# Kernel optimization log

Hardware: AMD Instinct MI355X
Metric: run time of the kernel (lower is better)

Reference implementation:

```python
import jax, jax.numpy as jnp
import numpy as np

# --- dims (match init_kwargs) ---
B = 2048          # batch
BACK = 512        # backcast_length (in_dim of first layer)
UNITS = 512       # hidden units
FORE = 128        # forecast_length
TH = FORE         # thetas_dim (nb_harmonics=None)
NL = 4            # num_block_layers
NUM = 5           # grid intervals
K = 3             # spline order
MINP = 1          # min_period
NCOEF = NUM + K   # 8 spline coefficients per edge


def _grid(in_dim):
    # extended uniform grid over [-1,1] with K extra knots each side -> NUM+2K+1 points
    h = 2.0 / NUM
    pts = (np.arange(-K, NUM + K + 1) * h - 1.0).astype(np.float32)
    return jnp.asarray(np.tile(pts[None, :], (in_dim, 1)))


def _bspline(x, grid):
    # x: (B, in_dim), grid: (in_dim, NUM+2K+1) -> (B, in_dim, NUM+K)
    xe = x[:, :, None]
    g = grid[None]
    v = ((xe >= g[:, :, :-1]) & (xe < g[:, :, 1:])).astype(x.dtype)
    for p in range(1, K + 1):  # Cox-de Boor recursion, K is small & static
        v = (xe - g[:, :, :-(p + 1)]) / (g[:, :, p:-1] - g[:, :, :-(p + 1)]) * v[:, :, :-1] \
          + (g[:, :, p + 1:] - xe) / (g[:, :, p + 1:] - g[:, :, 1:-p]) * v[:, :, 1:]
    return v


def _kan(x, grid, coef, sb, ssp):
    # y[b,o] = sum_i sb[i,o]*silu(x[b,i]) + sum_i ssp[i,o]*sum_k B[b,i,k]*coef[i,o,k]
    # (mask == ones; scale_sp folded into coef to avoid (B,in,out) intermediate)
    bsp = _bspline(x, grid)                          # (B, in, NCOEF)
    base = jax.nn.silu(x)                            # (B, in)
    return base @ sb + jnp.einsum('bik,iok->bo', bsp, coef * ssp[:, :, None])


def _seasonal_basis():
    T = BACK + FORE
    lin = np.linspace(0.0, (T - 1) / T, T)           # linspace(centered=False)
    bl, fl = lin[:BACK], lin[BACK:]
    p1 = p2 = TH // 2                                # TH even
    f1 = np.linspace(0.0, T / MINP, p1)
    f2 = np.linspace(0.0, T / MINP, p2)
    Sb = np.concatenate([np.cos(2 * np.pi * f1[:, None] * bl),
                         np.sin(2 * np.pi * f2[:, None] * bl)]).astype(np.float32)
    Sf = np.concatenate([np.cos(2 * np.pi * f1[:, None] * fl),
                         np.sin(2 * np.pi * f2[:, None] * fl)]).astype(np.float32)
    return jnp.asarray(Sb), jnp.asarray(Sf)          # (TH, BACK), (TH, FORE)


def setup_inputs() -> dict:
    key = jax.random.key(0)
    ks = jax.random.split(key, 8)
    x = jax.random.uniform(ks[0], (B, BACK), jnp.float32, -1.0, 1.0)
    # fc KAN layers: first maps BACK->UNITS, rest UNITS->UNITS; BACK==UNITS so stack
    coef_fc = 0.1 * jax.random.normal(ks[1], (NL, UNITS, UNITS, NCOEF), jnp.float32)
    sb_fc = 0.3 * jax.random.normal(ks[2], (NL, UNITS, UNITS), jnp.float32)
    ssp_fc = 1.0 + 0.1 * jax.random.normal(ks[3], (NL, UNITS, UNITS), jnp.float32)
    # shared theta layer UNITS -> TH
    coef_th = 0.1 * jax.random.normal(ks[4], (UNITS, TH, NCOEF), jnp.float32)
    sb_th = 0.3 * jax.random.normal(ks[5], (UNITS, TH), jnp.float32)
    ssp_th = 1.0 + 0.1 * jax.random.normal(ks[6], (UNITS, TH), jnp.float32)
    return dict(x=x, coef_fc=coef_fc, sb_fc=sb_fc, ssp_fc=ssp_fc,
                coef_th=coef_th, sb_th=sb_th, ssp_th=ssp_th)


def reference(x, coef_fc, sb_fc, ssp_fc, coef_th, sb_th, ssp_th):
    grid = _grid(UNITS)  # BACK == UNITS, one grid serves all layers
    h = x
    for l in range(NL):  # static small layer loop (dropout p=0 / eval)
        h = _kan(h, grid, coef_fc[l], sb_fc[l], ssp_fc[l])
    theta = _kan(h, grid, coef_th, sb_th, ssp_th)  # theta_b_fc is theta_f_fc (shared)
    Sb, Sf = _seasonal_basis()
    backcast = theta @ Sb    # (B, BACK)
    forecast = theta @ Sf    # (B, FORE)
    return backcast, forecast
```

## Files before the change

### kernel.cpp

```cpp
#include <hip/hip_runtime.h>
#include <stdint.h>


typedef unsigned short u16;
typedef __attribute__((ext_vector_type(8))) short short8;
typedef __attribute__((ext_vector_type(4))) float f32x4;

#define NB 2048
#define KD 4608
#define NTH 128
#define NTT 640

__device__ __forceinline__ u16 f2bf(float f) {
  union { float f; uint32_t u; } c; c.f = f;
  return (u16)((c.u + 0x7FFFu + ((c.u >> 16) & 1u)) >> 16);
}

__device__ __forceinline__ void load_lds16(const void* g, void* lds) {
  __builtin_amdgcn_global_load_lds((const __attribute__((address_space(1))) void*)g,
                                   (__attribute__((address_space(3))) void*)lds, 16, 0, 0);
}

__device__ __forceinline__ void bspline8(float x, float* v8) {
  float g[12];
  #pragma unroll
  for (int j = 0; j < 12; ++j) g[j] = (float)((j - 3) * 0.4 - 1.0);
  float w[11];
  #pragma unroll
  for (int j = 0; j < 11; ++j) w[j] = (x >= g[j] && x < g[j+1]) ? 1.0f : 0.0f;
  #pragma unroll
  for (int p = 1; p <= 3; ++p) {
    #pragma unroll
    for (int j = 0; j < 11 - p; ++j) {
      const float i1 = 1.0f / (g[j+p] - g[j]);
      const float i2 = 1.0f / (g[j+p+1] - g[j+1]);
      w[j] = (x - g[j]) * i1 * w[j] + (g[j+p+1] - x) * i2 * w[j+1];
    }
  }
  #pragma unroll
  for (int j = 0; j < 8; ++j) v8[j] = w[j];
}

__device__ __forceinline__ void expand_quad(const float* xv, u16* __restrict__ row, int i0) {
  float base[4], v[4][8];
  #pragma unroll
  for (int e = 0; e < 4; ++e) {
    base[e] = xv[e] / (1.0f + __expf(-xv[e]));
    bspline8(xv[e], v[e]);
  }
  short4 s;
  s.x = (short)f2bf(base[0]); s.y = (short)f2bf(base[1]);
  s.z = (short)f2bf(base[2]); s.w = (short)f2bf(base[3]);
  *(short4*)(row + i0) = s;
  #pragma unroll
  for (int f = 0; f < 8; ++f) {
    s.x = (short)f2bf(v[0][f]); s.y = (short)f2bf(v[1][f]);
    s.z = (short)f2bf(v[2][f]); s.w = (short)f2bf(v[3][f]);
    *(short4*)(row + (1 + f) * 512 + i0) = s;
  }
}

__global__ __launch_bounds__(256)
void setup_kernel(const float* __restrict__ coef_fc, const float* __restrict__ sb_fc,
                  const float* __restrict__ ssp_fc,  const float* __restrict__ coef_th,
                  const float* __restrict__ sb_th,   const float* __restrict__ ssp_th,
                  const float* __restrict__ x,
                  u16* __restrict__ WtFc, u16* __restrict__ WtTh,
                  float* __restrict__ S,  u16* __restrict__ Act) {
  const int blk = blockIdx.x, tid = threadIdx.x;
  __shared__ u16 T[9 * 64 * 66];
  if (blk < 272) {
    const float *coef, *sb, *ssp; u16* Wt; int O, l, i0, o0;
    if (blk < 256) {
      coef = coef_fc; sb = sb_fc; ssp = ssp_fc; Wt = WtFc; O = 512;
      l = blk >> 6; i0 = ((blk >> 3) & 7) * 64; o0 = (blk & 7) * 64;
    } else {
      coef = coef_th; sb = sb_th; ssp = ssp_th; Wt = WtTh; O = 128;
      const int t = blk - 256;
      l = 0; i0 = (t >> 1) * 64; o0 = (t & 1) * 64;
    }
    #pragma unroll 4
    for (int pass = 0; pass < 16; ++pass) {
      const int o_loc = tid & 63;
      const int i_loc = pass * 4 + (tid >> 6);
      const size_t io = ((size_t)l * 512 + i0 + i_loc) * (size_t)O + o0 + o_loc;
      const float sspv = ssp[io];
      const float4 a = *(const float4*)(coef + io * 8);
      const float4 b = *(const float4*)(coef + io * 8 + 4);
      u16* t0 = T + i_loc * 66 + o_loc;
      t0[0 * 64 * 66] = f2bf(sb[io]);
      t0[1 * 64 * 66] = f2bf(a.x * sspv);
      t0[2 * 64 * 66] = f2bf(a.y * sspv);
      t0[3 * 64 * 66] = f2bf(a.z * sspv);
      t0[4 * 64 * 66] = f2bf(a.w * sspv);
      t0[5 * 64 * 66] = f2bf(b.x * sspv);
      t0[6 * 64 * 66] = f2bf(b.y * sspv);
      t0[7 * 64 * 66] = f2bf(b.z * sspv);
      t0[8 * 64 * 66] = f2bf(b.w * sspv);
    }
    __syncthreads();
    #pragma unroll
    for (int f = 0; f < 9; ++f)
      #pragma unroll 4
      for (int pass = 0; pass < 16; ++pass) {
        const int i_loc = tid & 63;
        const int o_loc = pass * 4 + (tid >> 6);
        Wt[((size_t)l * O + o0 + o_loc) * KD + f * 512 + i0 + i_loc] =
            T[(f * 64 + i_loc) * 66 + o_loc];
      }
  } else if (blk < 292) {
    const int base = (blk - 272) * 4096;
    #pragma unroll 4
    for (int q = 0; q < 16; ++q) {
      const int id = base + q * 256 + tid;
      const int j = id & 127, t = id >> 7;
      const int m = ((j & 63) * t) % 63;
      const float ang = (float)(6.283185307179586 * (double)m / 63.0);
      S[(size_t)j * NTT + t] = (j < 64) ? cosf(ang) : sinf(ang);
    }
  } else {
    #pragma unroll
    for (int q = 0; q < 4; ++q) {
      const int qid = (blk - 292) * 1024 + q * 256 + tid;
      const int b = qid >> 7, i0 = (qid & 127) * 4;
      const float4 v = *(const float4*)(x + (size_t)qid * 4);
      float xv[4] = {v.x, v.y, v.z, v.w};
      expand_quad(xv, Act + (size_t)b * KD, i0);
    }
  }
}

template<int NSUM>
__global__ __launch_bounds__(256)
void expand_kernel(const float* __restrict__ src, u16* __restrict__ Act) {
  const int qid = blockIdx.x * 256 + threadIdx.x;
  const int b = qid >> 7, i0 = (qid & 127) * 4;
  float xv[4] = {0.f, 0.f, 0.f, 0.f};
  #pragma unroll
  for (int t = 0; t < NSUM; ++t) {
    const float4 v = *(const float4*)(src + (size_t)t * NB * 512 + (size_t)qid * 4);
    xv[0] += v.x; xv[1] += v.y; xv[2] += v.z; xv[3] += v.w;
  }
  expand_quad(xv, Act + (size_t)b * KD, i0);
}

__device__ __forceinline__ void stage_tile(const u16* __restrict__ A, const u16* __restrict__ Bt,
                                           u16* As, u16* Bs, int rowBase, int colBase,
                                           int kOff, int wave, int lane) {
  const int sRow   = lane >> 3;
  const int sChunk = (lane & 7) ^ sRow;
  #pragma unroll
  for (int j = 0; j < 4; ++j) {
    const int slot = (wave * 4 + j) * 8;
    load_lds16(A  + (size_t)(rowBase + slot + sRow) * KD + kOff + sChunk * 8, As + slot * 64);
    load_lds16(Bt + (size_t)(colBase + slot + sRow) * KD + kOff + sChunk * 8, Bs + slot * 64);
  }
}

__device__ __forceinline__ void mma_step(const u16* As, const u16* Bs, f32x4 acc[4][4],
                                         int wr, int wc, int lane) {
  const int lr = lane & 15, lk8 = lane >> 4;
  #pragma unroll
  for (int ks = 0; ks < 2; ++ks) {
    short8 af[4], bf[4];
    const int kc = ks * 4 + lk8;
    #pragma unroll
    for (int m = 0; m < 4; ++m) {
      const int r = wr * 64 + m * 16 + lr;
      af[m] = *(const short8*)(As + r * 64 + ((kc ^ (r & 7)) * 8));
    }
    #pragma unroll
    for (int n = 0; n < 4; ++n) {
      const int r = wc * 64 + n * 16 + lr;
      bf[n] = *(const short8*)(Bs + r * 64 + ((kc ^ (r & 7)) * 8));
    }
    #pragma unroll
    for (int m = 0; m < 4; ++m)
      #pragma unroll
      for (int n = 0; n < 4; ++n)
        acc[m][n] = __builtin_amdgcn_mfma_f32_16x16x32_bf16(af[m], bf[n], acc[m][n], 0, 0, 0);
  }
}

template<int N, int KITER>
__device__ __forceinline__ void gemm_body(const u16* __restrict__ A, const u16* __restrict__ Bt,
                                          float* __restrict__ Cp, int bx, int by, int bz,
                                          u16* sm) {
  const int tid  = threadIdx.x;
  const int wave = tid >> 6, lane = tid & 63;
  const int rowBase = bx * 128, colBase = by * 128;
  const int kb0 = bz * KITER;
  const int wr = wave >> 1, wc = wave & 1;

  u16 *Ac = sm,             *Bc = sm + 8192;
  u16 *An = sm + 2 * 8192,  *Bn = sm + 3 * 8192;
  u16 *Af = sm + 4 * 8192,  *Bf = sm + 5 * 8192;

  f32x4 acc[4][4] = {};

  stage_tile(A, Bt, Ac, Bc, rowBase, colBase, (kb0 + 0) * 64, wave, lane);
  stage_tile(A, Bt, An, Bn, rowBase, colBase, (kb0 + 1) * 64, wave, lane);

  for (int t = 0; t < KITER - 1; ++t) {
    asm volatile("s_waitcnt vmcnt(8)" ::: "memory");
    __builtin_amdgcn_s_barrier();
    if (t + 2 < KITER)
      stage_tile(A, Bt, Af, Bf, rowBase, colBase, (kb0 + t + 2) * 64, wave, lane);
    mma_step(Ac, Bc, acc, wr, wc, lane);
    __builtin_amdgcn_s_barrier();
    u16* tp;
    tp = Ac; Ac = An; An = Af; Af = tp;
    tp = Bc; Bc = Bn; Bn = Bf; Bf = tp;
  }
  asm volatile("s_waitcnt vmcnt(0)" ::: "memory");
  __builtin_amdgcn_s_barrier();
  mma_step(Ac, Bc, acc, wr, wc, lane);

  float* out = Cp + (size_t)bz * (size_t)NB * N;
  #pragma unroll
  for (int m = 0; m < 4; ++m) {
    const int row0 = rowBase + wr * 64 + m * 16 + (lane >> 4) * 4;
    #pragma unroll
    for (int n = 0; n < 4; ++n) {
      const int col = colBase + wc * 64 + n * 16 + (lane & 15);
      #pragma unroll
      for (int r = 0; r < 4; ++r)
        out[(size_t)(row0 + r) * N + col] = acc[m][n][r];
    }
  }
}

__global__ __launch_bounds__(256, 1)
void gemm_fc(const u16* __restrict__ A, const u16* __restrict__ Bt, float* __restrict__ Cp) {
  __shared__ __align__(16) u16 sm[6 * 8192];
  const int id  = blockIdx.x;
  const int xcd = id & 7;
  const int bz  = xcd >> 1;
  const int u   = id >> 3;
  const int bx  = ((u & 7) << 1) | (xcd & 1);
  const int by  = u >> 3;
  gemm_body<512, 18>(A, Bt, Cp, bx, by, bz, sm);
}

__global__ __launch_bounds__(256, 1)
void gemm_th(const u16* __restrict__ A, const u16* __restrict__ Bt, float* __restrict__ Cp) {
  __shared__ __align__(16) u16 sm[6 * 8192];
  gemm_body<NTH, 9>(A, Bt, Cp, blockIdx.x, 0, blockIdx.z, sm);
}

__global__ __launch_bounds__(256)
void proj_kernel(const float* __restrict__ Part, const float* __restrict__ S,
                 float* __restrict__ out) {
  __shared__ float Ts[64][129];
  const int tid = threadIdx.x;
  const int brow = blockIdx.x * 64, bcol = blockIdx.y * 64;
  for (int idx = tid; idx < 64 * 128; idx += 256) {
    const int r = idx >> 7, c = idx & 127;
    float s = 0.f;
    #pragma unroll
    for (int t = 0; t < 8; ++t)
      s += Part[(size_t)t * NB * NTH + (size_t)(brow + r) * NTH + c];
    Ts[r][c] = s;
  }
  __syncthreads();
  const int tx = tid & 15, ty = tid >> 4;
  const int r0 = ty * 4, c0 = tx * 4;
  float acc[4][4] = {};
  for (int k = 0; k < 128; ++k) {
    const float4 sv = *(const float4*)(S + (size_t)k * NTT + bcol + c0);
    #pragma unroll
    for (int rr = 0; rr < 4; ++rr) {
      const float tv = Ts[r0 + rr][k];
      acc[rr][0] += tv * sv.x; acc[rr][1] += tv * sv.y;
      acc[rr][2] += tv * sv.z; acc[rr][3] += tv * sv.w;
    }
  }
  #pragma unroll
  for (int rr = 0; rr < 4; ++rr) {
    const int b = brow + r0 + rr;
    #pragma unroll
    for (int cc = 0; cc < 4; ++cc) {
      const int t = bcol + c0 + cc;
      if (t < 512) out[(size_t)b * 512 + t] = acc[rr][cc];
      else         out[(size_t)NB * 512 + (size_t)b * NTH + (t - 512)] = acc[rr][cc];
    }
  }
}

extern "C" void kernel_launch(void* const* d_in, const int* in_sizes, int n_in,
                              void* d_out, int out_size, void* d_ws, size_t ws_size,
                              hipStream_t stream) {
  (void)in_sizes; (void)n_in; (void)out_size; (void)ws_size;
  const float* x       = (const float*)d_in[0];
  const float* coef_fc = (const float*)d_in[1];
  const float* sb_fc   = (const float*)d_in[2];
  const float* ssp_fc  = (const float*)d_in[3];
  const float* coef_th = (const float*)d_in[4];
  const float* sb_th   = (const float*)d_in[5];
  const float* ssp_th  = (const float*)d_in[6];
  float* out = (float*)d_out;

  u16*  WtFc = (u16*)d_ws;
  u16*  WtTh = WtFc + (size_t)4 * 512 * KD;
  u16*  Act  = WtTh + (size_t)NTH * KD;
  float* Part = (float*)(Act + (size_t)NB * KD);
  float* S    = Part + (size_t)4 * NB * 512;

  setup_kernel<<<dim3(548), dim3(256), 0, stream>>>(coef_fc, sb_fc, ssp_fc,
                                                    coef_th, sb_th, ssp_th, x,
                                                    WtFc, WtTh, S, Act);
  for (int l = 0; l < 4; ++l) {
    gemm_fc<<<dim3(256), dim3(256), 0, stream>>>(Act, WtFc + (size_t)l * 512 * KD, Part);
    expand_kernel<4><<<dim3(1024), dim3(256), 0, stream>>>(Part, Act);
  }
  gemm_th<<<dim3(16, 1, 8), dim3(256), 0, stream>>>(Act, WtTh, Part);
  proj_kernel<<<dim3(32, 10), dim3(256), 0, stream>>>(Part, S, out);
}
```

Baseline: 240.1 us.

## Fuse B-spline expansion into GEMM epilogue and drop split-K partials

```diff
diff --git a/kernel.cpp b/kernel.cpp
--- a/kernel.cpp
+++ b/kernel.cpp
@@ -130,137 +130,130 @@
   }
 }
 
-template<int NSUM>
-__global__ __launch_bounds__(256)
-void expand_kernel(const float* __restrict__ src, u16* __restrict__ Act) {
-  const int qid = blockIdx.x * 256 + threadIdx.x;
-  const int b = qid >> 7, i0 = (qid & 127) * 4;
-  float xv[4] = {0.f, 0.f, 0.f, 0.f};
-  #pragma unroll
-  for (int t = 0; t < NSUM; ++t) {
-    const float4 v = *(const float4*)(src + (size_t)t * NB * 512 + (size_t)qid * 4);
-    xv[0] += v.x; xv[1] += v.y; xv[2] += v.z; xv[3] += v.w;
-  }
-  expand_quad(xv, Act + (size_t)b * KD, i0);
-}
-
-__device__ __forceinline__ void stage_tile(const u16* __restrict__ A, const u16* __restrict__ Bt,
-                                           u16* As, u16* Bs, int rowBase, int colBase,
-                                           int kOff, int wave, int lane) {
+template<bool EXPAND>
+__global__ __launch_bounds__(512, 1)
+void gemm_fused(const u16* __restrict__ A, const u16* __restrict__ Bt,
+                u16* __restrict__ ActOut, float* __restrict__ ThOut) {
+  __shared__ __align__(16) u16 smb[3 * 8192];
+  __shared__ __align__(16) float Cl[64 * 68];
+  const int tid  = threadIdx.x;
+  const int wave = tid >> 6, lane = tid & 63;
+  int bx, by;
+  if (EXPAND) {
+    const int xcd = blockIdx.x & 7, j = blockIdx.x >> 3;
+    bx = xcd * 4 + (j & 3); by = j >> 2;
+  } else {
+    bx = blockIdx.x & 31; by = blockIdx.x >> 5;
+  }
+  const int rowBase = bx * 64, colBase = by * 64;
+  const int wr = wave >> 2, wc = wave & 3;
+
   const int sRow   = lane >> 3;
   const int sChunk = (lane & 7) ^ sRow;
-  #pragma unroll
-  for (int j = 0; j < 4; ++j) {
-    const int slot = (wave * 4 + j) * 8;
-    load_lds16(A  + (size_t)(rowBase + slot + sRow) * KD + kOff + sChunk * 8, As + slot * 64);
-    load_lds16(Bt + (size_t)(colBase + slot + sRow) * KD + kOff + sChunk * 8, Bs + slot * 64);
-  }
-}
-
-__device__ __forceinline__ void mma_step(const u16* As, const u16* Bs, f32x4 acc[4][4],
-                                         int wr, int wc, int lane) {
-  const int lr = lane & 15, lk8 = lane >> 4;
-  #pragma unroll
-  for (int ks = 0; ks < 2; ++ks) {
-    short8 af[4], bf[4];
-    const int kc = ks * 4 + lk8;
-    #pragma unroll
-    for (int m = 0; m < 4; ++m) {
-      const int r = wr * 64 + m * 16 + lr;
-      af[m] = *(const short8*)(As + r * 64 + ((kc ^ (r & 7)) * 8));
-    }
-    #pragma unroll
-    for (int n = 0; n < 4; ++n) {
-      const int r = wc * 64 + n * 16 + lr;
-      bf[n] = *(const short8*)(Bs + r * 64 + ((kc ^ (r & 7)) * 8));
-    }
-    #pragma unroll
-    for (int m = 0; m < 4; ++m)
+  const int slot   = wave * 8;
+
+  u16 *p0 = smb, *p1 = smb + 8192, *p2 = smb + 16384;
+  f32x4 acc[2] = {};
+
+  {
+    const u16* gA = A  + (size_t)(rowBase + slot + sRow) * KD + sChunk * 8;
+    const u16* gB = Bt + (size_t)(colBase + slot + sRow) * KD + sChunk * 8;
+    load_lds16(gA,      p0 + slot * 64);
+    load_lds16(gB,      p0 + 4096 + slot * 64);
+    load_lds16(gA + 64, p1 + slot * 64);
+    load_lds16(gB + 64, p1 + 4096 + slot * 64);
+  }
+
+  for (int t = 0; t < 71; ++t) {
+    asm volatile("s_waitcnt vmcnt(2)" ::: "memory");
+    __builtin_amdgcn_s_barrier();
+    if (t + 2 < 72) {
+      const int kOff = (t + 2) * 64;
+      load_lds16(A  + (size_t)(rowBase + slot + sRow) * KD + kOff + sChunk * 8,
+                 p2 + slot * 64);
+      load_lds16(Bt + (size_t)(colBase + slot + sRow) * KD + kOff + sChunk * 8,
+                 p2 + 4096 + slot * 64);
+    }
+    {
+      const u16* As = p0;
+      const u16* Bs = p0 + 4096;
       #pragma unroll
-      for (int n = 0; n < 4; ++n)
-        acc[m][n] = __builtin_amdgcn_mfma_f32_16x16x32_bf16(af[m], bf[n], acc[m][n], 0, 0, 0);
-  }
-}
-
-template<int N, int KITER>
-__device__ __forceinline__ void gemm_body(const u16* __restrict__ A, const u16* __restrict__ Bt,
-                                          float* __restrict__ Cp, int bx, int by, int bz,
-                                          u16* sm) {
-  const int tid  = threadIdx.x;
-  const int wave = tid >> 6, lane = tid & 63;
-  const int rowBase = bx * 128, colBase = by * 128;
-  const int kb0 = bz * KITER;
-  const int wr = wave >> 1, wc = wave & 1;
-
-  u16 *Ac = sm,             *Bc = sm + 8192;
-  u16 *An = sm + 2 * 8192,  *Bn = sm + 3 * 8192;
-  u16 *Af = sm + 4 * 8192,  *Bf = sm + 5 * 8192;
-
-  f32x4 acc[4][4] = {};
-
-  stage_tile(A, Bt, Ac, Bc, rowBase, colBase, (kb0 + 0) * 64, wave, lane);
-  stage_tile(A, Bt, An, Bn, rowBase, colBase, (kb0 + 1) * 64, wave, lane);
-
-  for (int t = 0; t < KITER - 1; ++t) {
-    asm volatile("s_waitcnt vmcnt(8)" ::: "memory");
+      for (int ks = 0; ks < 2; ++ks) {
+        const int kc = ks * 4 + (lane >> 4);
+        short8 af[2], bf;
+        #pragma unroll
+        for (int m = 0; m < 2; ++m) {
+          const int r = wr * 32 + m * 16 + (lane & 15);
+          af[m] = *(const short8*)(As + r * 64 + ((kc ^ (r & 7)) * 8));
+        }
+        {
+          const int r = wc * 16 + (lane & 15);
+          bf = *(const short8*)(Bs + r * 64 + ((kc ^ (r & 7)) * 8));
+        }
+        #pragma unroll
+        for (int m = 0; m < 2; ++m)
+          acc[m] = __builtin_amdgcn_mfma_f32_16x16x32_bf16(af[m], bf, acc[m], 0, 0, 0);
+      }
+    }
     __builtin_amdgcn_s_barrier();
-    if (t + 2 < KITER)
-      stage_tile(A, Bt, Af, Bf, rowBase, colBase, (kb0 + t + 2) * 64, wave, lane);
-    mma_step(Ac, Bc, acc, wr, wc, lane);
-    __builtin_amdgcn_s_barrier();
-    u16* tp;
-    tp = Ac; Ac = An; An = Af; Af = tp;
-    tp = Bc; Bc = Bn; Bn = Bf; Bf = tp;
+    u16* tp = p0; p0 = p1; p1 = p2; p2 = tp;
   }
   asm volatile("s_waitcnt vmcnt(0)" ::: "memory");
   __builtin_amdgcn_s_barrier();
-  mma_step(Ac, Bc, acc, wr, wc, lane);
-
-  float* out = Cp + (size_t)bz * (size_t)NB * N;
-  #pragma unroll
-  for (int m = 0; m < 4; ++m) {
-    const int row0 = rowBase + wr * 64 + m * 16 + (lane >> 4) * 4;
-    #pragma unroll
-    for (int n = 0; n < 4; ++n) {
-      const int col = colBase + wc * 64 + n * 16 + (lane & 15);
+  {
+    const u16* As = p0;
+    const u16* Bs = p0 + 4096;
+    #pragma unroll
+    for (int ks = 0; ks < 2; ++ks) {
+      const int kc = ks * 4 + (lane >> 4);
+      short8 af[2], bf;
       #pragma unroll
-      for (int r = 0; r < 4; ++r)
-        out[(size_t)(row0 + r) * N + col] = acc[m][n][r];
-    }
-  }
-}
-
-__global__ __launch_bounds__(256, 1)
-void gemm_fc(const u16* __restrict__ A, const u16* __restrict__ Bt, float* __restrict__ Cp) {
-  __shared__ __align__(16) u16 sm[6 * 8192];
-  const int id  = blockIdx.x;
-  const int xcd = id & 7;
-  const int bz  = xcd >> 1;
-  const int u   = id >> 3;
-  const int bx  = ((u & 7) << 1) | (xcd & 1);
-  const int by  = u >> 3;
-  gemm_body<512, 18>(A, Bt, Cp, bx, by, bz, sm);
-}
-
-__global__ __launch_bounds__(256, 1)
-void gemm_th(const u16* __restrict__ A, const u16* __restrict__ Bt, float* __restrict__ Cp) {
-  __shared__ __align__(16) u16 sm[6 * 8192];
-  gemm_body<NTH, 9>(A, Bt, Cp, blockIdx.x, 0, blockIdx.z, sm);
+      for (int m = 0; m < 2; ++m) {
+        const int r = wr * 32 + m * 16 + (lane & 15);
+        af[m] = *(const short8*)(As + r * 64 + ((kc ^ (r & 7)) * 8));
+      }
+      {
+        const int r = wc * 16 + (lane & 15);
+        bf = *(const short8*)(Bs + r * 64 + ((kc ^ (r & 7)) * 8));
+      }
+      #pragma unroll
+      for (int m = 0; m < 2; ++m)
+        acc[m] = __builtin_amdgcn_mfma_f32_16x16x32_bf16(af[m], bf, acc[m], 0, 0, 0);
+    }
+  }
+
+  #pragma unroll
+  for (int m = 0; m < 2; ++m) {
+    const int row = wr * 32 + m * 16 + (lane >> 4) * 4;
+    const int col = wc * 16 + (lane & 15);
+    #pragma unroll
+    for (int r = 0; r < 4; ++r)
+      Cl[(row + r) * 68 + col] = acc[m][r];
+  }
+  __syncthreads();
+  #pragma unroll
+  for (int pass = 0; pass < 2; ++pass) {
+    const int q = pass * 512 + tid;
+    const int b_loc = q >> 4, o4 = (q & 15) * 4;
+    const float4 v = *(const float4*)(Cl + b_loc * 68 + o4);
+    if (EXPAND) {
+      float xv[4] = {v.x, v.y, v.z, v.w};
+      expand_quad(xv, ActOut + (size_t)(rowBase + b_loc) * KD, colBase + o4);
+    } else {
+      *(float4*)(ThOut + (size_t)(rowBase + b_loc) * NTH + colBase + o4) = v;
+    }
+  }
 }
 
 __global__ __launch_bounds__(256)
-void proj_kernel(const float* __restrict__ Part, const float* __restrict__ S,
+void proj_kernel(const float* __restrict__ theta, const float* __restrict__ S,
                  float* __restrict__ out) {
   __shared__ float Ts[64][129];
   const int tid = threadIdx.x;
   const int brow = blockIdx.x * 64, bcol = blockIdx.y * 64;
   for (int idx = tid; idx < 64 * 128; idx += 256) {
     const int r = idx >> 7, c = idx & 127;
-    float s = 0.f;
-    #pragma unroll
-    for (int t = 0; t < 8; ++t)
-      s += Part[(size_t)t * NB * NTH + (size_t)(brow + r) * NTH + c];
-    Ts[r][c] = s;
+    Ts[r][c] = theta[(size_t)(brow + r) * NTH + c];
   }
   __syncthreads();
   const int tx = tid & 15, ty = tid >> 4;
@@ -300,19 +293,22 @@
   const float* ssp_th  = (const float*)d_in[6];
   float* out = (float*)d_out;
 
-  u16*  WtFc = (u16*)d_ws;
-  u16*  WtTh = WtFc + (size_t)4 * 512 * KD;
-  u16*  Act  = WtTh + (size_t)NTH * KD;
-  float* Part = (float*)(Act + (size_t)NB * KD);
-  float* S    = Part + (size_t)4 * NB * 512;
+  u16*  WtFc  = (u16*)d_ws;
+  u16*  WtTh  = WtFc + (size_t)4 * 512 * KD;
+  u16*  ActA  = WtTh + (size_t)NTH * KD;
+  u16*  ActB  = ActA + (size_t)NB * KD;
+  float* theta = (float*)(ActB + (size_t)NB * KD);
+  float* S     = theta + (size_t)NB * NTH;
 
   setup_kernel<<<dim3(548), dim3(256), 0, stream>>>(coef_fc, sb_fc, ssp_fc,
                                                     coef_th, sb_th, ssp_th, x,
-                                                    WtFc, WtTh, S, Act);
+                                                    WtFc, WtTh, S, ActA);
+  u16* Acur = ActA; u16* Anext = ActB;
   for (int l = 0; l < 4; ++l) {
-    gemm_fc<<<dim3(256), dim3(256), 0, stream>>>(Act, WtFc + (size_t)l * 512 * KD, Part);
-    expand_kernel<4><<<dim3(1024), dim3(256), 0, stream>>>(Part, Act);
-  }
-  gemm_th<<<dim3(16, 1, 8), dim3(256), 0, stream>>>(Act, WtTh, Part);
-  proj_kernel<<<dim3(32, 10), dim3(256), 0, stream>>>(Part, S, out);
-}
+    gemm_fused<true><<<dim3(256), dim3(512), 0, stream>>>(
+        Acur, WtFc + (size_t)l * 512 * KD, Anext, nullptr);
+    u16* tp = Acur; Acur = Anext; Anext = tp;
+  }
+  gemm_fused<false><<<dim3(64), dim3(512), 0, stream>>>(Acur, WtTh, nullptr, theta);
+  proj_kernel<<<dim3(32, 10), dim3(256), 0, stream>>>(theta, S, out);
+}
```

After: 254.0 us. 5.8% more time.
